# Kernel tuning notes

Measured on AMD Instinct MI355X. Metric: run time of the kernel, lower is better.

Reference implementation:

```python
import jax, jax.numpy as jnp
import numpy as np

B, S, D = 4, 2048, 1024
N_EXPERTS, EXPERT_SIZE = 16, 256
WIDTH = N_EXPERTS * EXPERT_SIZE  # 4096


def setup_inputs() -> dict:
    key = jax.random.key(0)
    k_x, k_w1, k_w2, k_g = jax.random.split(key, 4)
    x = jax.random.normal(k_x, (B, S, D), dtype=jnp.float32)
    # Linear params, fan-in scaled init
    w1 = jax.random.normal(k_w1, (D, WIDTH), dtype=jnp.float32) / np.sqrt(D).astype(np.float32)
    b1 = jnp.zeros((WIDTH,), dtype=jnp.float32)
    w2 = jax.random.normal(k_w2, (WIDTH, D), dtype=jnp.float32) / np.sqrt(WIDTH).astype(np.float32)
    b2 = jnp.zeros((D,), dtype=jnp.float32)
    return {"x": x, "w1": w1, "b1": b1, "w2": w2, "b2": b2}


def reference(x, w1, b1, w2, b2):
    # NOTE: the original module computes expert-choice routing tensors
    # (gate einsum -> topk -> one_hot -> identity matmul 'gather'), but the
    # returned value is ONLY the dense FFN applied to x; all routing results
    # are dead code with no effect on the output. Faithful output math:
    h = jax.nn.relu(jnp.einsum('bsd,dw->bsw', x, w1) + b1)  # [B,S,WIDTH]
    return jnp.einsum('bsw,wd->bsd', h, w2) + b2            # [B,S,D]
```

## Files before the change

kernel.cpp:

```cpp
#include <hip/hip_runtime.h>
#include <hip/hip_bf16.h>


typedef __bf16 bf16;
typedef __bf16 bf16x4 __attribute__((ext_vector_type(4)));
typedef __bf16 bf16x8 __attribute__((ext_vector_type(8)));
typedef float  f32x4  __attribute__((ext_vector_type(4)));

#define BM 128
#define BN 128
#define BK 64

__device__ __forceinline__ void gload_lds16(const bf16* g, bf16* l) {
    __builtin_amdgcn_global_load_lds(
        (const __attribute__((address_space(1))) unsigned int*)g,
        (__attribute__((address_space(3))) unsigned int*)l,
        16, 0, 0);
}

__global__ __launch_bounds__(256) void cast_f32_bf16(
    const float4* __restrict__ in, bf16x4* __restrict__ out, int n4)
{
    int i = blockIdx.x * 256 + threadIdx.x;
    if (i < n4) {
        float4 v = in[i];
        bf16x4 o;
        o.x = (bf16)v.x; o.y = (bf16)v.y; o.z = (bf16)v.z; o.w = (bf16)v.w;
        out[i] = o;
    }
}

__global__ __launch_bounds__(256) void transpose_cast(
    const float* __restrict__ in, bf16* __restrict__ out, int K, int N)
{
    __shared__ __align__(16) bf16 tile[64][72];
    const int k0 = blockIdx.y * 64;
    const int n0 = blockIdx.x * 64;
    const int t  = threadIdx.x;

    const int lr = t >> 4;
    const int lc = (t & 15) << 2;
#pragma unroll
    for (int p = 0; p < 4; ++p) {
        int k = p * 16 + lr;
        float4 v = *(const float4*)(in + (size_t)(k0 + k) * N + n0 + lc);
        tile[lc + 0][k] = (bf16)v.x;
        tile[lc + 1][k] = (bf16)v.y;
        tile[lc + 2][k] = (bf16)v.z;
        tile[lc + 3][k] = (bf16)v.w;
    }
    __syncthreads();

    const int wr = t >> 3;
    const int wc = (t & 7) << 3;
#pragma unroll
    for (int p = 0; p < 2; ++p) {
        int n = p * 32 + wr;
        *(bf16x8*)(out + (size_t)(n0 + n) * K + k0 + wc) =
            *(const bf16x8*)&tile[n][wc];
    }
}

template <int FUSE_RELU_BF16>
__global__ __launch_bounds__(256, 3) void gemm_bt(
    const bf16* __restrict__ A, const bf16* __restrict__ Bt,
    const float* __restrict__ bias, void* __restrict__ Cout,
    int M, int N, int K)
{
    __shared__ __align__(16) bf16 As[BM * BK];
    __shared__ __align__(16) bf16 Bs[BN * BK];

    const int tid  = threadIdx.x;
    const int wave = tid >> 6;
    const int lane = tid & 63;

    const int l8  = lane >> 3;
    const int c8  = lane & 7;
    const int swc = (c8 ^ l8) << 3;
    const size_t K_ = (size_t)K;

    const bf16* gA[4]; const bf16* gB[4];
    bf16* lA[4]; bf16* lB[4];
#pragma unroll
    for (int g = 0; g < 4; ++g) {
        const int rr = wave * 32 + g * 8 + l8;
        gA[g] = A  + ((size_t)blockIdx.y * BM + rr) * K_ + swc;
        gB[g] = Bt + ((size_t)blockIdx.x * BN + rr) * K_ + swc;
        lA[g] = &As[(wave * 32 + g * 8) * BK] + lane * 8;
        lB[g] = &Bs[(wave * 32 + g * 8) * BK] + lane * 8;
    }

    const int wm   = (wave >> 1) << 6;
    const int wn   = (wave & 1) << 6;
    const int quad = lane >> 4;
    const int r    = lane & 15;
    const int r7   = lane & 7;

    f32x4 acc[4][4] = {};

    for (int k0 = 0; k0 < K; k0 += BK) {
        __syncthreads();
#pragma unroll
        for (int g = 0; g < 4; ++g) {
            gload_lds16(gA[g], lA[g]);
            gload_lds16(gB[g], lB[g]);
            gA[g] += BK; gB[g] += BK;
        }
        __syncthreads();

#pragma unroll
        for (int h = 0; h < 2; ++h) {
            const int ch = ((h * 4 + quad) ^ r7) << 3;
            bf16x8 af[4], bfr[4];
#pragma unroll
            for (int i = 0; i < 4; ++i)
                af[i] = *(const bf16x8*)&As[(wm + i * 16 + r) * BK + ch];
#pragma unroll
            for (int j = 0; j < 4; ++j)
                bfr[j] = *(const bf16x8*)&Bs[(wn + j * 16 + r) * BK + ch];
#pragma unroll
            for (int i = 0; i < 4; ++i)
#pragma unroll
                for (int j = 0; j < 4; ++j)
                    acc[i][j] = __builtin_amdgcn_mfma_f32_16x16x32_bf16(
                        af[i], bfr[j], acc[i][j], 0, 0, 0);
        }
    }

    const int m_base = blockIdx.y * BM + wm + quad * 4;
    const int n_base = blockIdx.x * BN + wn + r;
    float bv[4];
#pragma unroll
    for (int j = 0; j < 4; ++j) bv[j] = bias[n_base + j * 16];

    if (FUSE_RELU_BF16) {
        bf16* Cb = (bf16*)Cout;
#pragma unroll
        for (int i = 0; i < 4; ++i) {
#pragma unroll
            for (int p = 0; p < 4; ++p) {
                size_t row = (size_t)(m_base + i * 16 + p) * (size_t)N;
#pragma unroll
                for (int j = 0; j < 4; ++j) {
                    float v = acc[i][j][p] + bv[j];
                    v = v > 0.f ? v : 0.f;
                    Cb[row + n_base + j * 16] = (bf16)v;
                }
            }
        }
    } else {
        float* Cf = (float*)Cout;
#pragma unroll
        for (int i = 0; i < 4; ++i) {
#pragma unroll
            for (int p = 0; p < 4; ++p) {
                size_t row = (size_t)(m_base + i * 16 + p) * (size_t)N;
#pragma unroll
                for (int j = 0; j < 4; ++j) {
                    Cf[row + n_base + j * 16] = acc[i][j][p] + bv[j];
                }
            }
        }
    }
}

extern "C" void kernel_launch(void* const* d_in, const int* in_sizes, int n_in,
                              void* d_out, int out_size, void* d_ws, size_t ws_size,
                              hipStream_t stream)
{
    const float* x  = (const float*)d_in[0];
    const float* w1 = (const float*)d_in[1];
    const float* b1 = (const float*)d_in[2];
    const float* w2 = (const float*)d_in[3];
    const float* b2 = (const float*)d_in[4];
    float* out = (float*)d_out;

    const int M = 8192, D = 1024, W = 4096;

    char* ws = (char*)d_ws;
    bf16* xb  = (bf16*)(ws);
    bf16* w1t = (bf16*)(ws + (size_t)(16 << 20));
    bf16* w2t = (bf16*)(ws + (size_t)(24 << 20));
    bf16* h   = (bf16*)(ws + (size_t)(32 << 20));

    {
        int n4 = (M * D) / 4;
        cast_f32_bf16<<<(n4 + 255) / 256, 256, 0, stream>>>(
            (const float4*)x, (bf16x4*)xb, n4);
    }
    transpose_cast<<<dim3(W / 64, D / 64), 256, 0, stream>>>(w1, w1t, D, W);
    transpose_cast<<<dim3(D / 64, W / 64), 256, 0, stream>>>(w2, w2t, W, D);

    gemm_bt<1><<<dim3(W / BN, M / BM), 256, 0, stream>>>(
        xb, w1t, b1, (void*)h, M, W, D);

    gemm_bt<0><<<dim3(D / BN, M / BM), 256, 0, stream>>>(
        h, w2t, b2, (void*)out, M, D, W);
}
```

Measured before the change: 252.5 us.

## Double-buffer GEMM LDS loads, remap blocks per XCD, and fuse prep kernels

Splits the GEMM's shared-memory tiles into two buffers so the next K-tile's global-to-LDS load is issued while the current tile is computed, with occupancy hint lowered to 2 blocks per CU to fit the larger LDS footprint. Block IDs are remapped to a 1D grid so that blocks on the same XCD share A rows for L2 reuse. The three cast/transpose kernels are merged into one launch to cut launch overhead. Risks are lower occupancy and the double-buffered loop assuming an even number of K-tiles.

```diff
diff --git a/kernel.cpp b/kernel.cpp
--- a/kernel.cpp
+++ b/kernel.cpp
@@ -18,26 +18,12 @@
         16, 0, 0);
 }
 
-__global__ __launch_bounds__(256) void cast_f32_bf16(
-    const float4* __restrict__ in, bf16x4* __restrict__ out, int n4)
-{
-    int i = blockIdx.x * 256 + threadIdx.x;
-    if (i < n4) {
-        float4 v = in[i];
-        bf16x4 o;
-        o.x = (bf16)v.x; o.y = (bf16)v.y; o.z = (bf16)v.z; o.w = (bf16)v.w;
-        out[i] = o;
-    }
-}
-
-__global__ __launch_bounds__(256) void transpose_cast(
-    const float* __restrict__ in, bf16* __restrict__ out, int K, int N)
-{
-    __shared__ __align__(16) bf16 tile[64][72];
-    const int k0 = blockIdx.y * 64;
-    const int n0 = blockIdx.x * 64;
-    const int t  = threadIdx.x;
-
+__device__ __forceinline__ void transpose_tile(
+    const float* __restrict__ in, bf16* __restrict__ out,
+    int K, int N, int bx, int by, int t, bf16 (*tile)[72])
+{
+    const int k0 = by * 64;
+    const int n0 = bx * 64;
     const int lr = t >> 4;
     const int lc = (t & 15) << 2;
 #pragma unroll
@@ -50,7 +36,6 @@
         tile[lc + 3][k] = (bf16)v.w;
     }
     __syncthreads();
-
     const int wr = t >> 3;
     const int wc = (t & 7) << 3;
 #pragma unroll
@@ -61,14 +46,43 @@
     }
 }
 
+__global__ __launch_bounds__(256) void prep(
+    const float* __restrict__ x,  bf16* __restrict__ xb,
+    const float* __restrict__ w1, bf16* __restrict__ w1t,
+    const float* __restrict__ w2, bf16* __restrict__ w2t)
+{
+    __shared__ __align__(16) bf16 tile[64][72];
+    const int b = blockIdx.x;
+    const int t = threadIdx.x;
+    if (b < 8192) {
+        int i = b * 256 + t;
+        float4 v = ((const float4*)x)[i];
+        bf16x4 o;
+        o.x = (bf16)v.x; o.y = (bf16)v.y; o.z = (bf16)v.z; o.w = (bf16)v.w;
+        ((bf16x4*)xb)[i] = o;
+    } else if (b < 9216) {
+        int b2 = b - 8192;
+        transpose_tile(w1, w1t, 1024, 4096, b2 & 63, b2 >> 6, t, tile);
+    } else {
+        int b2 = b - 9216;
+        transpose_tile(w2, w2t, 4096, 1024, b2 & 15, b2 >> 4, t, tile);
+    }
+}
+
 template <int FUSE_RELU_BF16>
-__global__ __launch_bounds__(256, 3) void gemm_bt(
+__global__ __launch_bounds__(256, 2) void gemm_bt(
     const bf16* __restrict__ A, const bf16* __restrict__ Bt,
     const float* __restrict__ bias, void* __restrict__ Cout,
-    int M, int N, int K)
-{
-    __shared__ __align__(16) bf16 As[BM * BK];
-    __shared__ __align__(16) bf16 Bs[BN * BK];
+    int M, int N, int K, int nx)
+{
+    __shared__ __align__(16) bf16 As[2][BM * BK];
+    __shared__ __align__(16) bf16 Bs[2][BN * BK];
+
+    const int lid = blockIdx.x;
+    const int xcd = lid & 7;
+    const int j   = lid >> 3;
+    const int bx  = j % nx;
+    const int by  = (j / nx) * 8 + xcd;
 
     const int tid  = threadIdx.x;
     const int wave = tid >> 6;
@@ -80,15 +94,13 @@
     const size_t K_ = (size_t)K;
 
     const bf16* gA[4]; const bf16* gB[4];
-    bf16* lA[4]; bf16* lB[4];
 #pragma unroll
     for (int g = 0; g < 4; ++g) {
         const int rr = wave * 32 + g * 8 + l8;
-        gA[g] = A  + ((size_t)blockIdx.y * BM + rr) * K_ + swc;
-        gB[g] = Bt + ((size_t)blockIdx.x * BN + rr) * K_ + swc;
-        lA[g] = &As[(wave * 32 + g * 8) * BK] + lane * 8;
-        lB[g] = &Bs[(wave * 32 + g * 8) * BK] + lane * 8;
-    }
+        gA[g] = A  + ((size_t)by * BM + rr) * K_ + swc;
+        gB[g] = Bt + ((size_t)bx * BN + rr) * K_ + swc;
+    }
+    const int lofs = (wave * 32) * BK + lane * 8;
 
     const int wm   = (wave >> 1) << 6;
     const int wn   = (wave & 1) << 6;
@@ -98,40 +110,50 @@
 
     f32x4 acc[4][4] = {};
 
-    for (int k0 = 0; k0 < K; k0 += BK) {
-        __syncthreads();
+    auto stage = [&](int buf) {
 #pragma unroll
         for (int g = 0; g < 4; ++g) {
-            gload_lds16(gA[g], lA[g]);
-            gload_lds16(gB[g], lB[g]);
+            gload_lds16(gA[g], &As[buf][lofs + g * (8 * BK)]);
+            gload_lds16(gB[g], &Bs[buf][lofs + g * (8 * BK)]);
             gA[g] += BK; gB[g] += BK;
         }
-        __syncthreads();
-
+    };
+    auto compute = [&](int buf) {
 #pragma unroll
         for (int h = 0; h < 2; ++h) {
             const int ch = ((h * 4 + quad) ^ r7) << 3;
             bf16x8 af[4], bfr[4];
 #pragma unroll
             for (int i = 0; i < 4; ++i)
-                af[i] = *(const bf16x8*)&As[(wm + i * 16 + r) * BK + ch];
-#pragma unroll
-            for (int j = 0; j < 4; ++j)
-                bfr[j] = *(const bf16x8*)&Bs[(wn + j * 16 + r) * BK + ch];
+                af[i] = *(const bf16x8*)&As[buf][(wm + i * 16 + r) * BK + ch];
+#pragma unroll
+            for (int jj = 0; jj < 4; ++jj)
+                bfr[jj] = *(const bf16x8*)&Bs[buf][(wn + jj * 16 + r) * BK + ch];
 #pragma unroll
             for (int i = 0; i < 4; ++i)
 #pragma unroll
-                for (int j = 0; j < 4; ++j)
-                    acc[i][j] = __builtin_amdgcn_mfma_f32_16x16x32_bf16(
-                        af[i], bfr[j], acc[i][j], 0, 0, 0);
-        }
-    }
-
-    const int m_base = blockIdx.y * BM + wm + quad * 4;
-    const int n_base = blockIdx.x * BN + wn + r;
+                for (int jj = 0; jj < 4; ++jj)
+                    acc[i][jj] = __builtin_amdgcn_mfma_f32_16x16x32_bf16(
+                        af[i], bfr[jj], acc[i][jj], 0, 0, 0);
+        }
+    };
+
+    const int T = K / BK;
+    stage(0);
+    for (int t = 0; t < T; t += 2) {
+        __syncthreads();
+        stage(1);
+        compute(0);
+        __syncthreads();
+        if (t + 2 < T) stage(0);
+        compute(1);
+    }
+
+    const int m_base = by * BM + wm + quad * 4;
+    const int n_base = bx * BN + wn + r;
     float bv[4];
 #pragma unroll
-    for (int j = 0; j < 4; ++j) bv[j] = bias[n_base + j * 16];
+    for (int jj = 0; jj < 4; ++jj) bv[jj] = bias[n_base + jj * 16];
 
     if (FUSE_RELU_BF16) {
         bf16* Cb = (bf16*)Cout;
@@ -141,10 +163,10 @@
             for (int p = 0; p < 4; ++p) {
                 size_t row = (size_t)(m_base + i * 16 + p) * (size_t)N;
 #pragma unroll
-                for (int j = 0; j < 4; ++j) {
-                    float v = acc[i][j][p] + bv[j];
+                for (int jj = 0; jj < 4; ++jj) {
+                    float v = acc[i][jj][p] + bv[jj];
                     v = v > 0.f ? v : 0.f;
-                    Cb[row + n_base + j * 16] = (bf16)v;
+                    Cb[row + n_base + jj * 16] = (bf16)v;
                 }
             }
         }
@@ -156,8 +178,8 @@
             for (int p = 0; p < 4; ++p) {
                 size_t row = (size_t)(m_base + i * 16 + p) * (size_t)N;
 #pragma unroll
-                for (int j = 0; j < 4; ++j) {
-                    Cf[row + n_base + j * 16] = acc[i][j][p] + bv[j];
+                for (int jj = 0; jj < 4; ++jj) {
+                    Cf[row + n_base + jj * 16] = acc[i][jj][p] + bv[jj];
                 }
             }
         }
@@ -183,17 +205,11 @@
     bf16* w2t = (bf16*)(ws + (size_t)(24 << 20));
     bf16* h   = (bf16*)(ws + (size_t)(32 << 20));
 
-    {
-        int n4 = (M * D) / 4;
-        cast_f32_bf16<<<(n4 + 255) / 256, 256, 0, stream>>>(
-            (const float4*)x, (bf16x4*)xb, n4);
-    }
-    transpose_cast<<<dim3(W / 64, D / 64), 256, 0, stream>>>(w1, w1t, D, W);
-    transpose_cast<<<dim3(D / 64, W / 64), 256, 0, stream>>>(w2, w2t, W, D);
-
-    gemm_bt<1><<<dim3(W / BN, M / BM), 256, 0, stream>>>(
-        xb, w1t, b1, (void*)h, M, W, D);
-
-    gemm_bt<0><<<dim3(D / BN, M / BM), 256, 0, stream>>>(
-        h, w2t, b2, (void*)out, M, D, W);
-}
+    prep<<<8192 + 1024 + 1024, 256, 0, stream>>>(x, xb, w1, w1t, w2, w2t);
+
+    gemm_bt<1><<<(W / BN) * (M / BM), 256, 0, stream>>>(
+        xb, w1t, b1, (void*)h, M, W, D, W / BN);
+
+    gemm_bt<0><<<(D / BN) * (M / BM), 256, 0, stream>>>(
+        h, w2t, b2, (void*)out, M, D, W, D / BN);
+}
```

After: 268.0 us. +6.1%, slower.
